# Optimization experiments

Measured on AMD Instinct MI355X. Metric: run time of the kernel, lower is better.

## Reference

```python
import jax, jax.numpy as jnp
import numpy as np

DIM = 64
K = 8192
EPS = 1e-5


def setup_inputs() -> dict:
    key = jax.random.key(0)
    k1, k2, k3 = jax.random.split(key, 3)
    x = jax.random.normal(k1, (8, 4096, DIM), dtype=jnp.float32)
    mask = jnp.ones((8, 4096), dtype=bool)
    # frozen buffer: randn(K, D) * D**-0.5
    frozen_codebook = jax.random.normal(k2, (K, DIM), dtype=jnp.float32) * DIM ** -0.5
    # nn.Linear(D, D, bias=False) weight, shape (out, in) = (DIM, DIM)
    W = jax.random.normal(k3, (DIM, DIM), dtype=jnp.float32) * DIM ** -0.5
    return {"x": x, "mask": mask, "frozen_codebook": frozen_codebook, "W": W}


def reference(x, mask, frozen_codebook, W):
    # implicit codebook = Linear(frozen_codebook): [K, D]
    codebook = frozen_codebook @ W.T
    D = x.shape[-1]
    xf = x.reshape(-1, D)  # [N, D]
    mf = mask.reshape(-1)
    sq = jnp.sum(codebook * codebook, axis=-1)[None, :] - 2.0 * (xf @ codebook.T)  # [N, K]
    indices = jnp.argmin(jax.lax.stop_gradient(sq), axis=-1)  # [N]
    quantized = codebook[indices]  # embedding gather, [N, D]
    diff = quantized - xf
    dist_magnitude = jnp.linalg.norm(diff, axis=-1, keepdims=True)  # [N, 1]
    dist_magnitude = dist_magnitude * mf[:, None].astype(dist_magnitude.dtype)
    direction = diff / jnp.maximum(dist_magnitude, EPS)
    # DiVeQ trick: magnitude carries gradient, direction is detached
    quantized_out = xf + dist_magnitude * jax.lax.stop_gradient(direction)
    quantized_out = quantized_out.reshape(x.shape)
    indices = indices.reshape(x.shape[:-1])
    loss = jnp.asarray(0.0, dtype=x.dtype)
    return quantized_out, indices, loss
```

## Files before the change

kernel.cpp:

```cpp
#include <hip/hip_runtime.h>
#include <math.h>
#include <float.h>


#define DIM    64
#define KCODES 8192
#define NROWS  32768
#define EPSQ   1e-5f
#define NCHUNK 16
#define KCHUNK (KCODES / NCHUNK)
#define SUBS   (KCHUNK / 16)
#define RT     8

typedef _Float16 half8   __attribute__((ext_vector_type(8)));
typedef float    floatx4 __attribute__((ext_vector_type(4)));


__global__ __launch_bounds__(256) void cb_prep(const float* __restrict__ frozen,
                                               const float* __restrict__ W,
                                               _Float16* __restrict__ chg,
                                               _Float16* __restrict__ clg,
                                               float* __restrict__ gh) {
    __shared__ float Wl[DIM * 65];
    __shared__ float fz[4 * DIM];
    const int tid = threadIdx.x;

    for (int i = tid; i < DIM * DIM; i += 256) {
        int d = i >> 6, j = i & 63;
        Wl[d * 65 + j] = W[i];
    }
    const int kbase = blockIdx.x * 4;
    fz[tid] = frozen[kbase * DIM + tid];
    __syncthreads();

    const int kl = tid >> 6;
    const int d  = tid & 63;
    float dot = 0.f;
#pragma unroll
    for (int j = 0; j < DIM; j++)
        dot = fmaf(fz[kl * DIM + j], Wl[d * 65 + j], dot);

    const int k = kbase + kl;
    const int s = k >> 4, col = k & 15, j = d >> 3, e = d & 7;
    const size_t off = ((size_t)(s * 8 + j) * 16 + col) * 8 + e;
    _Float16 h = (_Float16)dot;
    chg[off] = h;
    clg[off] = (_Float16)(dot - (float)h);

    float ssum = dot * dot;
#pragma unroll
    for (int offx = 32; offx >= 1; offx >>= 1)
        ssum += __shfl_xor(ssum, offx, 64);
    if (d == 0) gh[k] = 0.5f * ssum;
}

__global__ __launch_bounds__(256, 2) void dist_argmin_mfma(
        const float* __restrict__ x,
        const _Float16* __restrict__ chg,
        const _Float16* __restrict__ clg,
        const float* __restrict__ gh,
        float* __restrict__ pd,
        float* __restrict__ pif) {
    const int tid  = threadIdx.x;
    const int wave = tid >> 6, lane = tid & 63;
    const int col  = lane & 15, quad = lane >> 4;
    const int rowblock = blockIdx.x * (RT * 16 * 4);
    const int chunk    = blockIdx.y;
    const int k0       = chunk * KCHUNK;

    const _Float16* cb_h = chg + (size_t)k0 * DIM;
    const _Float16* cb_l = clg + (size_t)k0 * DIM;
    const float*    ghp  = gh + k0;

    half8 axh[RT][2], axl[RT][2];
#pragma unroll
    for (int rt = 0; rt < RT; rt++) {
        const int row = rowblock + wave * (RT * 16) + rt * 16 + col;
        const floatx4* px = (const floatx4*)(x + (size_t)row * DIM);
#pragma unroll
        for (int h = 0; h < 2; h++) {
            floatx4 f0 = px[(h * 4 + quad) * 2];
            floatx4 f1 = px[(h * 4 + quad) * 2 + 1];
            half8 hi, lo;
#pragma unroll
            for (int jj = 0; jj < 4; jj++) {
                float v = f0[jj]; _Float16 hh = (_Float16)v;
                hi[jj] = hh; lo[jj] = (_Float16)(v - (float)hh);
            }
#pragma unroll
            for (int jj = 0; jj < 4; jj++) {
                float v = f1[jj]; _Float16 hh = (_Float16)v;
                hi[4 + jj] = hh; lo[4 + jj] = (_Float16)(v - (float)hh);
            }
            axh[rt][h] = hi; axl[rt][h] = lo;
        }
    }

    float best[RT][4];
    int   bsub[RT][4];
#pragma unroll
    for (int rt = 0; rt < RT; rt++)
#pragma unroll
        for (int r = 0; r < 4; r++) { best[rt][r] = -FLT_MAX; bsub[rt][r] = 0; }

    struct Frag { half8 h0, h1, l0, l1; float gv; };

    auto load_frag = [&](int s) -> Frag {
        Frag f;
        const _Float16* b = cb_h + (size_t)s * 1024;
        const _Float16* l = cb_l + (size_t)s * 1024;
        f.h0 = *(const half8*)(b + lane * 8);
        f.h1 = *(const half8*)(b + 512 + lane * 8);
        f.l0 = *(const half8*)(l + lane * 8);
        f.l1 = *(const half8*)(l + 512 + lane * 8);
        f.gv = ghp[s * 16 + col];
        return f;
    };

    auto compute_sub = [&](const Frag& f, int s) {
        const float ngv = -f.gv;
        const floatx4 cinit = {ngv, ngv, ngv, ngv};
#pragma unroll
        for (int rt = 0; rt < RT; rt++) {
            floatx4 acc;
            acc = __builtin_amdgcn_mfma_f32_16x16x32_f16(axh[rt][0], f.h0, cinit, 0, 0, 0);
            acc = __builtin_amdgcn_mfma_f32_16x16x32_f16(axh[rt][1], f.h1, acc, 0, 0, 0);
            acc = __builtin_amdgcn_mfma_f32_16x16x32_f16(axl[rt][0], f.h0, acc, 0, 0, 0);
            acc = __builtin_amdgcn_mfma_f32_16x16x32_f16(axl[rt][1], f.h1, acc, 0, 0, 0);
            acc = __builtin_amdgcn_mfma_f32_16x16x32_f16(axh[rt][0], f.l0, acc, 0, 0, 0);
            acc = __builtin_amdgcn_mfma_f32_16x16x32_f16(axh[rt][1], f.l1, acc, 0, 0, 0);
#pragma unroll
            for (int r = 0; r < 4; r++) {
                bool gt = acc[r] > best[rt][r];
                best[rt][r] = gt ? acc[r] : best[rt][r];
                bsub[rt][r] = gt ? s : bsub[rt][r];
            }
        }
    };

    Frag fa = load_frag(0);
    Frag fb = load_frag(1);
    for (int s = 0; s < SUBS; s += 2) {
        compute_sub(fa, s);
        fa = load_frag((s + 2) & (SUBS - 1));
        compute_sub(fb, s + 1);
        fb = load_frag((s + 3) & (SUBS - 1));
    }

#pragma unroll
    for (int rt = 0; rt < RT; rt++)
#pragma unroll
        for (int r = 0; r < 4; r++) {
            float v  = best[rt][r];
            float ix = (float)(bsub[rt][r] * 16 + col);
#pragma unroll
            for (int off = 8; off >= 1; off >>= 1) {
                float v2 = __shfl_xor(v, off, 16);
                float i2 = __shfl_xor(ix, off, 16);
                if (v2 > v || (v2 == v && i2 < ix)) { v = v2; ix = i2; }
            }
            if (col == 0) {
                const int row = rowblock + wave * (RT * 16) + rt * 16 + quad * 4 + r;
                pd [(size_t)chunk * NROWS + row] = -v;
                pif[(size_t)chunk * NROWS + row] = (float)k0 + ix;
            }
        }
}

__global__ __launch_bounds__(256) void finalize(const float* __restrict__ x,
                                                const _Float16* __restrict__ chg,
                                                const _Float16* __restrict__ clg,
                                                const float* __restrict__ pd,
                                                const float* __restrict__ pif,
                                                float* __restrict__ out) {
    const int row = blockIdx.x * 256 + threadIdx.x;

    float best = pd[row];
    float bix  = pif[row];
#pragma unroll
    for (int c = 1; c < NCHUNK; c++) {
        float d2 = pd[(size_t)c * NROWS + row];
        float i2 = pif[(size_t)c * NROWS + row];
        if (d2 < best) { best = d2; bix = i2; }
    }
    const int bidx = (int)bix;

    float xr[DIM];
    const floatx4* xp = (const floatx4*)(x + (size_t)row * DIM);
#pragma unroll
    for (int i = 0; i < DIM / 4; i++) {
        floatx4 v = xp[i];
#pragma unroll
        for (int jj = 0; jj < 4; jj++) xr[i * 4 + jj] = v[jj];
    }

    const int s = bidx >> 4, cc = bidx & 15;
    float diff[DIM], ss = 0.f;
#pragma unroll
    for (int j = 0; j < 8; j++) {
        const size_t off = ((size_t)(s * 8 + j) * 16 + cc) * 8;
        half8 hh = *(const half8*)(chg + off);
        half8 ll = *(const half8*)(clg + off);
#pragma unroll
        for (int e = 0; e < 8; e++) {
            const int d = j * 8 + e;
            diff[d] = ((float)hh[e] + (float)ll[e]) - xr[d];
        }
    }
#pragma unroll
    for (int d = 0; d < DIM; d++) ss = fmaf(diff[d], diff[d], ss);

    const float dist = sqrtf(ss);
    const float dm   = fmaxf(dist, EPSQ);
    floatx4* op = (floatx4*)(out + (size_t)row * DIM);
#pragma unroll
    for (int i = 0; i < DIM / 4; i++) {
        floatx4 o;
#pragma unroll
        for (int jj = 0; jj < 4; jj++)
            o[jj] = fmaf(dist, diff[i * 4 + jj] / dm, xr[i * 4 + jj]);
        op[i] = o;
    }
    out[(size_t)NROWS * DIM + row] = (float)bidx;
    if (row == 0) out[(size_t)NROWS * DIM + NROWS] = 0.f;
}

extern "C" void kernel_launch(void* const* d_in, const int* in_sizes, int n_in,
                              void* d_out, int out_size, void* d_ws, size_t ws_size,
                              hipStream_t stream) {
    const float* x      = (const float*)d_in[0];
    const float* frozen = (const float*)d_in[2];
    const float* W      = (const float*)d_in[3];
    float* out = (float*)d_out;

    char* ws = (char*)d_ws;
    _Float16* chg = (_Float16*)ws;
    _Float16* clg = chg + (size_t)KCODES * DIM;
    float*    gh  = (float*)(ws + 2u * KCODES * DIM * sizeof(_Float16));
    float*    pd  = gh + KCODES;
    float*    pif = pd + (size_t)NCHUNK * NROWS;

    cb_prep<<<KCODES / 4, 256, 0, stream>>>(frozen, W, chg, clg, gh);
    dist_argmin_mfma<<<dim3(NROWS / 512, NCHUNK), 256, 0, stream>>>(x, chg, clg, gh, pd, pif);
    finalize<<<NROWS / 256, 256, 0, stream>>>(x, chg, clg, pd, pif, out);
}
```

Before: 188.8 us.

## Fuse finalize into distance kernel via last-block atomic counter, regrid to single-wave blocks

Merges the finalize pass into the distance/argmin kernel. Each row group counts finished K-chunks with an atomic counter, and the last-arriving block reduces the partial minima and writes the quantized output. The grid changes to 64-thread blocks with 4 row tiles and 8 K-chunks instead of 16, giving more blocks with less work each. This removes a kernel launch and the partial-result round trip between kernels, at the cost of threadfence/atomic overhead, a serialized tail per row group, and a counter that is reset inside cb_prep.

```diff
diff --git a/kernel.cpp b/kernel.cpp
--- a/kernel.cpp
+++ b/kernel.cpp
@@ -7,10 +7,11 @@
 #define KCODES 8192
 #define NROWS  32768
 #define EPSQ   1e-5f
-#define NCHUNK 16
+#define NCHUNK 8
 #define KCHUNK (KCODES / NCHUNK)
 #define SUBS   (KCHUNK / 16)
-#define RT     8
+#define RT     4
+#define NROWB  (NROWS / 64)
 
 typedef _Float16 half8   __attribute__((ext_vector_type(8)));
 typedef float    floatx4 __attribute__((ext_vector_type(4)));
@@ -20,10 +21,13 @@
                                                const float* __restrict__ W,
                                                _Float16* __restrict__ chg,
                                                _Float16* __restrict__ clg,
-                                               float* __restrict__ gh) {
+                                               float* __restrict__ gh,
+                                               int* __restrict__ cnt) {
     __shared__ float Wl[DIM * 65];
     __shared__ float fz[4 * DIM];
     const int tid = threadIdx.x;
+
+    if (blockIdx.x < NROWB && tid == 0) cnt[blockIdx.x] = 0;
 
     for (int i = tid; i < DIM * DIM; i += 256) {
         int d = i >> 6, j = i & 63;
@@ -54,19 +58,21 @@
     if (d == 0) gh[k] = 0.5f * ssum;
 }
 
-__global__ __launch_bounds__(256, 2) void dist_argmin_mfma(
+__global__ __launch_bounds__(64, 3) void dist_fused(
         const float* __restrict__ x,
         const _Float16* __restrict__ chg,
         const _Float16* __restrict__ clg,
         const float* __restrict__ gh,
         float* __restrict__ pd,
-        float* __restrict__ pif) {
-    const int tid  = threadIdx.x;
-    const int wave = tid >> 6, lane = tid & 63;
+        float* __restrict__ pif,
+        int* __restrict__ cnt,
+        float* __restrict__ out) {
+    const int lane = threadIdx.x;
     const int col  = lane & 15, quad = lane >> 4;
-    const int rowblock = blockIdx.x * (RT * 16 * 4);
-    const int chunk    = blockIdx.y;
-    const int k0       = chunk * KCHUNK;
+    const int rowg    = blockIdx.x;
+    const int rowbase = rowg * 64;
+    const int chunk   = blockIdx.y;
+    const int k0      = chunk * KCHUNK;
 
     const _Float16* cb_h = chg + (size_t)k0 * DIM;
     const _Float16* cb_l = clg + (size_t)k0 * DIM;
@@ -75,7 +81,7 @@
     half8 axh[RT][2], axl[RT][2];
 #pragma unroll
     for (int rt = 0; rt < RT; rt++) {
-        const int row = rowblock + wave * (RT * 16) + rt * 16 + col;
+        const int row = rowbase + rt * 16 + col;
         const floatx4* px = (const floatx4*)(x + (size_t)row * DIM);
 #pragma unroll
         for (int h = 0; h < 2; h++) {
@@ -160,69 +166,69 @@
                 if (v2 > v || (v2 == v && i2 < ix)) { v = v2; ix = i2; }
             }
             if (col == 0) {
-                const int row = rowblock + wave * (RT * 16) + rt * 16 + quad * 4 + r;
+                const int row = rowbase + rt * 16 + quad * 4 + r;
                 pd [(size_t)chunk * NROWS + row] = -v;
                 pif[(size_t)chunk * NROWS + row] = (float)k0 + ix;
             }
         }
-}
-
-__global__ __launch_bounds__(256) void finalize(const float* __restrict__ x,
-                                                const _Float16* __restrict__ chg,
-                                                const _Float16* __restrict__ clg,
-                                                const float* __restrict__ pd,
-                                                const float* __restrict__ pif,
-                                                float* __restrict__ out) {
-    const int row = blockIdx.x * 256 + threadIdx.x;
-
-    float best = pd[row];
-    float bix  = pif[row];
+
+    __threadfence();
+    int old = 0;
+    if (lane == 0) old = atomicAdd(&cnt[rowg], 1);
+    old = __shfl(old, 0);
+    if (old != NCHUNK - 1) return;
+    __threadfence();
+
+    const int row = rowbase + lane;
+    float bsc = pd[row];
+    float bix = pif[row];
 #pragma unroll
     for (int c = 1; c < NCHUNK; c++) {
         float d2 = pd[(size_t)c * NROWS + row];
         float i2 = pif[(size_t)c * NROWS + row];
-        if (d2 < best) { best = d2; bix = i2; }
+        if (d2 < bsc) { bsc = d2; bix = i2; }
     }
     const int bidx = (int)bix;
-
-    float xr[DIM];
-    const floatx4* xp = (const floatx4*)(x + (size_t)row * DIM);
-#pragma unroll
-    for (int i = 0; i < DIM / 4; i++) {
-        floatx4 v = xp[i];
-#pragma unroll
-        for (int jj = 0; jj < 4; jj++) xr[i * 4 + jj] = v[jj];
-    }
-
-    const int s = bidx >> 4, cc = bidx & 15;
-    float diff[DIM], ss = 0.f;
+    const int bs = bidx >> 4, bc = bidx & 15;
+
+    float ss = 0.f;
 #pragma unroll
     for (int j = 0; j < 8; j++) {
-        const size_t off = ((size_t)(s * 8 + j) * 16 + cc) * 8;
+        const size_t off = ((size_t)(bs * 8 + j) * 16 + bc) * 8;
         half8 hh = *(const half8*)(chg + off);
         half8 ll = *(const half8*)(clg + off);
+        const float* xv = x + (size_t)row * DIM + j * 8;
 #pragma unroll
         for (int e = 0; e < 8; e++) {
-            const int d = j * 8 + e;
-            diff[d] = ((float)hh[e] + (float)ll[e]) - xr[d];
-        }
-    }
-#pragma unroll
-    for (int d = 0; d < DIM; d++) ss = fmaf(diff[d], diff[d], ss);
-
-    const float dist = sqrtf(ss);
-    const float dm   = fmaxf(dist, EPSQ);
-    floatx4* op = (floatx4*)(out + (size_t)row * DIM);
-#pragma unroll
-    for (int i = 0; i < DIM / 4; i++) {
-        floatx4 o;
-#pragma unroll
-        for (int jj = 0; jj < 4; jj++)
-            o[jj] = fmaf(dist, diff[i * 4 + jj] / dm, xr[i * 4 + jj]);
-        op[i] = o;
+            float df = ((float)hh[e] + (float)ll[e]) - xv[e];
+            ss = fmaf(df, df, ss);
+        }
+    }
+    const float dist  = sqrtf(ss);
+    const float scale = dist / fmaxf(dist, EPSQ);
+
+#pragma unroll
+    for (int j = 0; j < 8; j++) {
+        const size_t off = ((size_t)(bs * 8 + j) * 16 + bc) * 8;
+        half8 hh = *(const half8*)(chg + off);
+        half8 ll = *(const half8*)(clg + off);
+        const float* xv = x + (size_t)row * DIM + j * 8;
+        floatx4 o0, o1;
+#pragma unroll
+        for (int e = 0; e < 4; e++) {
+            float df = ((float)hh[e] + (float)ll[e]) - xv[e];
+            o0[e] = fmaf(scale, df, xv[e]);
+        }
+#pragma unroll
+        for (int e = 0; e < 4; e++) {
+            float df = ((float)hh[4 + e] + (float)ll[4 + e]) - xv[4 + e];
+            o1[e] = fmaf(scale, df, xv[4 + e]);
+        }
+        floatx4* op = (floatx4*)(out + (size_t)row * DIM + j * 8);
+        op[0] = o0; op[1] = o1;
     }
     out[(size_t)NROWS * DIM + row] = (float)bidx;
-    if (row == 0) out[(size_t)NROWS * DIM + NROWS] = 0.f;
+    if (rowg == 0 && lane == 0) out[(size_t)NROWS * DIM + NROWS] = 0.f;
 }
 
 extern "C" void kernel_launch(void* const* d_in, const int* in_sizes, int n_in,
@@ -239,8 +245,8 @@
     float*    gh  = (float*)(ws + 2u * KCODES * DIM * sizeof(_Float16));
     float*    pd  = gh + KCODES;
     float*    pif = pd + (size_t)NCHUNK * NROWS;
-
-    cb_prep<<<KCODES / 4, 256, 0, stream>>>(frozen, W, chg, clg, gh);
-    dist_argmin_mfma<<<dim3(NROWS / 512, NCHUNK), 256, 0, stream>>>(x, chg, clg, gh, pd, pif);
-    finalize<<<NROWS / 256, 256, 0, stream>>>(x, chg, clg, pd, pif, out);
+    int*      cnt = (int*)(pif + (size_t)NCHUNK * NROWS);
+
+    cb_prep<<<KCODES / 4, 256, 0, stream>>>(frozen, W, chg, clg, gh, cnt);
+    dist_fused<<<dim3(NROWB, NCHUNK), 64, 0, stream>>>(x, chg, clg, gh, pd, pif, cnt, out);
 }
```

Result: slower. 274.7 us (+45.5%).
